# Performance work log

Measured on AMD Instinct MI355X. Metric: run time of the kernel, lower is better.

The kernel has to match this reference:

```python
import jax, jax.numpy as jnp
import numpy as np

D = 32  # per-modality feature dim (hard-coded in module)


def setup_inputs() -> dict:
    key = jax.random.key(0)
    ks = jax.random.split(key, 6)
    B, U = 16, 2048
    return {
        "a_emb": jax.random.normal(ks[0], (B, U, D), dtype=jnp.float32),
        "v_emb": jax.random.normal(ks[1], (B, U, D), dtype=jnp.float32),
        "l_emb": jax.random.normal(ks[2], (B, U, D), dtype=jnp.float32),
        "fc1_w": jax.random.normal(ks[3], (2 * D, 2 * D), dtype=jnp.float32) * 0.1,
        "fc1_b": jax.random.normal(ks[4], (2 * D,), dtype=jnp.float32) * 0.1,
        "fc2_w": jax.random.normal(ks[5], (1, 2 * D), dtype=jnp.float32) * 0.1,
    }


def _bi_attn(f1, f2):
    # f1: [B,u1,d], f2: [B,u2,d]
    B12 = jnp.einsum("bid,bjd->bij", f1, f2)          # [B,u1,u2]
    N1 = jax.nn.softmax(B12, axis=1)                    # softmax over dim=1 (as in torch code)
    N2 = jax.nn.softmax(jnp.swapaxes(B12, 1, 2), axis=1)  # B21 = B12^T
    O1 = jnp.einsum("bij,bjd->bid", N1, f2)            # [B,u1,d]
    O2 = jnp.einsum("bji,bjd->bid", jnp.swapaxes(N2, 1, 2), f1)  # [B,u2,d]
    A1 = O1 * f1
    A2 = O2 * f2
    return jnp.concatenate([A1, A2], axis=2)            # [B,u,2d]


def reference(a_emb, v_emb, l_emb, fc1_w, fc1_b, fc2_w):
    attnAV = _bi_attn(a_emb, v_emb)
    attnAL = _bi_attn(a_emb, l_emb)
    attnVL = _bi_attn(v_emb, l_emb)
    u = a_emb.shape[1]
    # The original loop recomputes the identical Bi/Ci/alpha/CCA_i every iteration
    # (always slices index 0), so compute once and repeat u times.
    Bi = jnp.concatenate(
        [attnAV[:, 0:1, :], attnAL[:, 0:1, :], attnVL[:, 0:1, :]], axis=1
    )  # [B,3,2d]
    Ci = jnp.tanh(Bi @ fc1_w.T + fc1_b) @ fc2_w.T       # [B,3,1]
    alpha = jax.nn.softmax(Ci, axis=0)                   # softmax over batch dim (as in source)
    CCA_i = jnp.einsum("bki,bkd->bid", alpha, Bi)       # [B,1,2d]
    CCA = jnp.repeat(CCA_i, u, axis=1)                   # [B,u,2d]
    return CCA
```

## Files before the change

### kernel.cpp

```cpp
#include <hip/hip_runtime.h>

#define UU 2048
#define DM 32
#define TB 128
#define NB 16
#define NP 3
#define NT (UU / TB)
#define NSTRIP 16
#define ASZ (NB * UU * DM)

#define WS_S1 0
#define WS_S2 (NP * NB * UU)
#define WS_OO (2 * NP * NB * UU)
#define WS_CCA (WS_OO + NP * NB * 2 * DM)
#define WS_SPLIT 204800

typedef short short8_t __attribute__((ext_vector_type(8)));
typedef float float4_t __attribute__((ext_vector_type(4)));

#if __has_builtin(__builtin_amdgcn_exp2f)
#define EXP2(x) __builtin_amdgcn_exp2f(x)
#else
#define EXP2(x) exp2f(x)
#endif

#define SQRT_LOG2E 1.2011224087864498f

__device__ inline void async16(void* lds, const void* g) {
  __builtin_amdgcn_global_load_lds(
      (const __attribute__((address_space(1))) unsigned int*)g,
      (__attribute__((address_space(3))) unsigned int*)lds, 16, 0, 0);
}

__device__ inline void split8s(const float4 x0, const float4 x1, short8_t& h,
                               short8_t& lo) {
  float xs[8] = {x0.x, x0.y, x0.z, x0.w, x1.x, x1.y, x1.z, x1.w};
#pragma unroll
  for (int i = 0; i < 8; ++i) {
    float xv = xs[i] * SQRT_LOG2E;
    unsigned u = __float_as_uint(xv);
    h[i] = (short)(u >> 16);
    float hif = __uint_as_float(u & 0xffff0000u);
    lo[i] = (short)(__float_as_uint(xv - hif) >> 16);
  }
}

__global__ __launch_bounds__(256) void stage0_prep(
    const float* __restrict__ a, const float* __restrict__ v,
    const float* __restrict__ l, float* __restrict__ ws) {
  const int gid = blockIdx.x * 256 + threadIdx.x;
  if (gid < (NP * NB * 2 * DM) / 4)
    ((float4*)(ws + WS_OO))[gid] = make_float4(0.f, 0.f, 0.f, 0.f);

  const int per = ASZ / 8;
  const int arr = (gid >= per) + (gid >= 2 * per);
  const float* src = (arr == 0) ? a : (arr == 1) ? v : l;
  const int loc = gid - arr * per;
  const float4* sp = (const float4*)(src + (size_t)loc * 8);
  float4 x0 = sp[0], x1 = sp[1];
  short8_t h, lo;
  split8s(x0, x1, h, lo);
  unsigned short* hq =
      (unsigned short*)(ws + WS_SPLIT) + (size_t)arr * 2 * ASZ + (size_t)loc * 8;
  *(short8_t*)hq = h;
  *(short8_t*)(hq + ASZ) = lo;
}

__global__ __launch_bounds__(256, 3) void stage1_sums(
    const unsigned short* __restrict__ H, float* __restrict__ S1part,
    float* __restrict__ S2) {
  const int lid = blockIdx.x;
  const int xcd = lid & 7;
  const int r6 = lid >> 3;
  const int z = xcd * 6 + (r6 >> 4);
  const int strip = r6 & 15;
  const int p = z >> 4, b = z & 15;
  const int i0 = strip * TB;

  const int a1 = (p == 2) ? 1 : 0;
  const int a2 = (p == 0) ? 1 : 2;
  const unsigned short* f1h = H + (size_t)a1 * 2 * ASZ + (size_t)b * UU * DM;
  const unsigned short* f2h = H + (size_t)a2 * 2 * ASZ + (size_t)b * UU * DM;

  __shared__ __align__(16) unsigned short Bbuf[2][2][TB][DM];
  __shared__ float ldsC[4][TB];
  __shared__ float S1L[UU];

  const int t = threadIdx.x;
  const int lane = t & 63, w = t >> 6;
  const int lm = lane & 15, lq = lane >> 4, k0 = lq * 8;

#pragma unroll
  for (int m = 0; m < 8; ++m) S1L[m * 256 + t] = 0.f;

  short8_t a_h[2], a_l[2];
  {
    const unsigned short* ar = f1h + (size_t)(i0 + w * 32 + lm) * DM + k0;
    a_h[0] = *(const short8_t*)ar;
    a_h[1] = *(const short8_t*)(ar + 16 * DM);
    a_l[0] = *(const short8_t*)(ar + ASZ);
    a_l[1] = *(const short8_t*)(ar + ASZ + 16 * DM);
  }

  float rowp[2][4];
#pragma unroll
  for (int rt = 0; rt < 2; ++rt)
#pragma unroll
    for (int r = 0; r < 4; ++r) rowp[rt][r] = 0.f;

  auto stageB = [&](int buf, int jt) {
    const unsigned short* gh = f2h + (size_t)(jt * TB + w * 32) * DM + lane * 8;
    async16(&Bbuf[buf][0][w * 32][0], gh);
    async16(&Bbuf[buf][0][w * 32 + 16][0], gh + 16 * DM);
    async16(&Bbuf[buf][1][w * 32][0], gh + ASZ);
    async16(&Bbuf[buf][1][w * 32 + 16][0], gh + ASZ + 16 * DM);
  };

  auto compute = [&](int buf, int jt) {
    float colp[8];
#pragma unroll
    for (int ct = 0; ct < 8; ++ct) colp[ct] = 0.f;
#pragma unroll
    for (int ct = 0; ct < 8; ++ct) {
      short8_t b_h = *(const short8_t*)&Bbuf[buf][0][ct * 16 + lm][k0];
      short8_t b_l = *(const short8_t*)&Bbuf[buf][1][ct * 16 + lm][k0];
#pragma unroll
      for (int rt = 0; rt < 2; ++rt) {
        float4_t c = {0.f, 0.f, 0.f, 0.f};
        c = __builtin_amdgcn_mfma_f32_16x16x32_bf16(a_h[rt], b_h, c, 0, 0, 0);
        c = __builtin_amdgcn_mfma_f32_16x16x32_bf16(a_h[rt], b_l, c, 0, 0, 0);
        c = __builtin_amdgcn_mfma_f32_16x16x32_bf16(a_l[rt], b_h, c, 0, 0, 0);
        float e0 = EXP2(c[0]);
        float e1 = EXP2(c[1]);
        float e2 = EXP2(c[2]);
        float e3 = EXP2(c[3]);
        rowp[rt][0] += e0;
        rowp[rt][1] += e1;
        rowp[rt][2] += e2;
        rowp[rt][3] += e3;
        colp[ct] += (e0 + e1) + (e2 + e3);
      }
    }
#pragma unroll
    for (int ct = 0; ct < 8; ++ct) {
      float vv = colp[ct];
      vv += __shfl_xor(vv, 16, 64);
      vv += __shfl_xor(vv, 32, 64);
      if (lane < 16) ldsC[w][ct * 16 + lane] = vv;
    }
    asm volatile("s_waitcnt lgkmcnt(0)" ::: "memory");
    __builtin_amdgcn_s_barrier();
    asm volatile("" ::: "memory");
    if (t < TB)
      S1L[jt * TB + t] += ldsC[0][t] + ldsC[1][t] + ldsC[2][t] + ldsC[3][t];
  };

  stageB(0, 0);

#pragma unroll 2
  for (int k = 0; k < NT; ++k) {
    if (k + 1 < NT) {
      stageB((k + 1) & 1, k + 1);
      asm volatile("s_waitcnt vmcnt(4)" ::: "memory");
    } else {
      asm volatile("s_waitcnt vmcnt(0)" ::: "memory");
    }
    __builtin_amdgcn_s_barrier();
    asm volatile("" ::: "memory");
    compute(k & 1, k);
  }
  __syncthreads();

  {
    float* dst = S1part + ((size_t)z * NSTRIP + strip) * UU;
#pragma unroll
    for (int m = 0; m < 8; ++m) dst[m * 256 + t] = S1L[m * 256 + t];
  }
  const size_t base = (size_t)z * UU;
#pragma unroll
  for (int rt = 0; rt < 2; ++rt)
#pragma unroll
    for (int r = 0; r < 4; ++r) {
      float vv = rowp[rt][r];
      vv += __shfl_xor(vv, 1, 64);
      vv += __shfl_xor(vv, 2, 64);
      vv += __shfl_xor(vv, 4, 64);
      vv += __shfl_xor(vv, 8, 64);
      if (lm == 0) S2[base + i0 + w * 32 + rt * 16 + lq * 4 + r] = vv;
    }
}

__global__ __launch_bounds__(256) void stage2_O(
    const float* __restrict__ a, const float* __restrict__ v,
    const float* __restrict__ l, const float* __restrict__ S1part,
    const float* __restrict__ S2, float* __restrict__ OO) {
  const int idx = blockIdx.x;
  const int chunk = idx & 7;
  const int pd = idx >> 3;
  const int dir = pd & 1;
  const int pb = pd >> 1;
  const int p = pb >> 4, b = pb & 15;
  const float* f1 = (p == 2) ? v : a;
  const float* f2 = (p == 0) ? v : l;
  f1 += (size_t)b * UU * DM;
  f2 += (size_t)b * UU * DM;
  const float* qrow = (dir == 0) ? f1 : f2;
  const float* rows = (dir == 0) ? f2 : f1;

  __shared__ float qv[DM];
  __shared__ __align__(16) float rowsL[256 * 36];
  __shared__ float wL[256];
  __shared__ float wred[8][DM];
  const int t = threadIdx.x;
  if (t < DM) qv[t] = qrow[t];
  __syncthreads();

  const int r = chunk * 256 + t;
  const float4* rp = (const float4*)(rows + (size_t)r * DM);
  float dot = 0.f;
#pragma unroll
  for (int qq = 0; qq < 8; ++qq) {
    float4 x = rp[qq];
    *(float4*)&rowsL[t * 36 + qq * 4] = x;
    dot = fmaf(x.x, qv[4 * qq + 0], dot);
    dot = fmaf(x.y, qv[4 * qq + 1], dot);
    dot = fmaf(x.z, qv[4 * qq + 2], dot);
    dot = fmaf(x.w, qv[4 * qq + 3], dot);
  }
  float den;
  if (dir == 0) {
    const float* sp = S1part + (size_t)pb * NSTRIP * UU + r;
    float s = 0.f;
#pragma unroll
    for (int s16 = 0; s16 < NSTRIP; ++s16) s += sp[(size_t)s16 * UU];
    den = s;
  } else {
    den = S2[(size_t)pb * UU + r];
  }
  wL[t] = __expf(dot) / den;
  __syncthreads();

  const int d = t & 31, sl = t >> 5;
  float acc = 0.f;
#pragma unroll
  for (int k = 0; k < 32; ++k) {
    const int rr = sl * 32 + k;
    acc = fmaf(wL[rr], rowsL[rr * 36 + d], acc);
  }
  wred[sl][d] = acc;
  __syncthreads();
  if (t < DM) {
    float o = 0.f;
#pragma unroll
    for (int s2 = 0; s2 < 8; ++s2) o += wred[s2][t];
    atomicAdd(&OO[(size_t)pd * DM + t], o);
  }
}

__global__ __launch_bounds__(1024) void stage3_head(
    const float* __restrict__ a, const float* __restrict__ v,
    const float* __restrict__ l, const float* __restrict__ OO,
    const float* __restrict__ fc1w, const float* __restrict__ fc1b,
    const float* __restrict__ fc2w, float* __restrict__ CCA) {
  const int t = threadIdx.x;
  __shared__ float BiL[NB * NP * 64];
  __shared__ float CiS[NB * NP];
  __shared__ float denomk[NP];
  __shared__ float fwL[64 * 65];

#pragma unroll
  for (int it = 0; it < 4; ++it) {
    int m = it * 1024 + t;
    fwL[(m >> 6) * 65 + (m & 63)] = fc1w[m];
  }

#pragma unroll
  for (int iter = 0; iter < 3; ++iter) {
    int m = iter * 1024 + t;
    int bk = m >> 6;
    int h = m & 63;
    int b = bk / NP, p = bk - b * NP;
    int dir = h >> 5, hd = h & 31;
    const float* base = (dir == 0) ? ((p == 2) ? v : a) : ((p == 0) ? v : l);
    float q = base[(size_t)b * UU * DM + hd];
    int pb = p * NB + b;
    BiL[bk * 64 + h] = OO[(pb * 2 + dir) * DM + hd] * q;
  }
  __syncthreads();

  const int h = t & 63;
  const int g = t >> 6;
#pragma unroll
  for (int iter = 0; iter < 3; ++iter) {
    int bk = g + 16 * iter;
    float x = fc1b[h];
#pragma unroll 8
    for (int c = 0; c < 64; ++c)
      x = fmaf(BiL[bk * 64 + c], fwL[h * 65 + c], x);
    float vv = tanhf(x) * fc2w[h];
#pragma unroll
    for (int off = 32; off > 0; off >>= 1) vv += __shfl_down(vv, off, 64);
    if (h == 0) CiS[bk] = vv;
  }
  __syncthreads();

  if (t < NP) {
    float s = 0.f;
    for (int b = 0; b < NB; ++b) s += __expf(CiS[b * NP + t]);
    denomk[t] = s;
  }
  __syncthreads();

  {
    int b = g;
    float s = 0.f;
#pragma unroll
    for (int k = 0; k < NP; ++k)
      s += __expf(CiS[b * NP + k]) / denomk[k] * BiL[(b * NP + k) * 64 + h];
    CCA[b * 64 + h] = s;
  }
}

__global__ __launch_bounds__(256) void stage4_bcast(
    const float* __restrict__ CCA, float4* __restrict__ out) {
  const int gid = blockIdx.x * 256 + threadIdx.x;
  const int c4 = gid & 15;
  const int b = gid >> 15;
  const float4* cc = (const float4*)CCA;
  out[gid] = cc[b * 16 + c4];
}

extern "C" void kernel_launch(void* const* d_in, const int* in_sizes, int n_in,
                              void* d_out, int out_size, void* d_ws,
                              size_t ws_size, hipStream_t stream) {
  const float* a = (const float*)d_in[0];
  const float* v = (const float*)d_in[1];
  const float* l = (const float*)d_in[2];
  const float* fc1w = (const float*)d_in[3];
  const float* fc1b = (const float*)d_in[4];
  const float* fc2w = (const float*)d_in[5];
  float* out = (float*)d_out;

  float* ws = (float*)d_ws;
  float* S2 = ws + WS_S2;
  float* OO = ws + WS_OO;
  float* CCA = ws + WS_CCA;
  const unsigned short* H = (const unsigned short*)(ws + WS_SPLIT);
  float* S1part = (float*)d_out;

  stage0_prep<<<dim3(1536), 256, 0, stream>>>(a, v, l, ws);
  stage1_sums<<<dim3(NP * NB * NSTRIP), 256, 0, stream>>>(H, S1part, S2);
  stage2_O<<<dim3(NP * NB * 2 * 8), 256, 0, stream>>>(a, v, l, S1part, S2, OO);
  stage3_head<<<dim3(1), 1024, 0, stream>>>(a, v, l, OO, fc1w, fc1b, fc2w,
                                            CCA);
  stage4_bcast<<<dim3(2048), 256, 0, stream>>>(CCA, (float4*)out);
}
```

Before: 147.1 us.

## Split stage1 work by column tile per wave to drop per-tile barriers

Stage1 previously gave each wave 32 rows of the query strip and staged shared B tiles through LDS with async loads, needing a block barrier every tile to combine column sums. Now each wave holds all 128 query rows in registers and loads its own 32 B columns straight from global memory into registers, double-buffered. Each wave then owns distinct S1L entries, so the per-tile barrier and LDS reduction go away, and a single final LDS reduction combines row sums across waves. This raises register pressure (8 A fragments plus 8x4 row accumulators) and drops LDS reuse of B across waves, which may hurt occupancy under launch_bounds(256,3).

```diff
diff --git a/kernel.cpp b/kernel.cpp
--- a/kernel.cpp
+++ b/kernel.cpp
@@ -25,12 +25,6 @@
 #endif
 
 #define SQRT_LOG2E 1.2011224087864498f
-
-__device__ inline void async16(void* lds, const void* g) {
-  __builtin_amdgcn_global_load_lds(
-      (const __attribute__((address_space(1))) unsigned int*)g,
-      (__attribute__((address_space(3))) unsigned int*)lds, 16, 0, 0);
-}
 
 __device__ inline void split8s(const float4 x0, const float4 x1, short8_t& h,
                                short8_t& lo) {
@@ -82,50 +76,55 @@
   const unsigned short* f1h = H + (size_t)a1 * 2 * ASZ + (size_t)b * UU * DM;
   const unsigned short* f2h = H + (size_t)a2 * 2 * ASZ + (size_t)b * UU * DM;
 
-  __shared__ __align__(16) unsigned short Bbuf[2][2][TB][DM];
-  __shared__ float ldsC[4][TB];
   __shared__ float S1L[UU];
+  __shared__ float S2L[4][TB];
 
   const int t = threadIdx.x;
   const int lane = t & 63, w = t >> 6;
   const int lm = lane & 15, lq = lane >> 4, k0 = lq * 8;
 
 #pragma unroll
-  for (int m = 0; m < 8; ++m) S1L[m * 256 + t] = 0.f;
-
-  short8_t a_h[2], a_l[2];
-  {
-    const unsigned short* ar = f1h + (size_t)(i0 + w * 32 + lm) * DM + k0;
-    a_h[0] = *(const short8_t*)ar;
-    a_h[1] = *(const short8_t*)(ar + 16 * DM);
-    a_l[0] = *(const short8_t*)(ar + ASZ);
-    a_l[1] = *(const short8_t*)(ar + ASZ + 16 * DM);
-  }
-
-  float rowp[2][4];
-#pragma unroll
-  for (int rt = 0; rt < 2; ++rt)
+  for (int m = 0; m < 8; ++m) {
+    int jt = m * 2 + (lane >> 5);
+    S1L[jt * TB + w * 32 + (lane & 31)] = 0.f;
+  }
+
+  short8_t a_h[8], a_l[8];
+#pragma unroll
+  for (int rt = 0; rt < 8; ++rt) {
+    const unsigned short* ar = f1h + (size_t)(i0 + rt * 16 + lm) * DM + k0;
+    a_h[rt] = *(const short8_t*)ar;
+    a_l[rt] = *(const short8_t*)(ar + ASZ);
+  }
+
+  float rowp[8][4];
+#pragma unroll
+  for (int rt = 0; rt < 8; ++rt)
 #pragma unroll
     for (int r = 0; r < 4; ++r) rowp[rt][r] = 0.f;
 
-  auto stageB = [&](int buf, int jt) {
-    const unsigned short* gh = f2h + (size_t)(jt * TB + w * 32) * DM + lane * 8;
-    async16(&Bbuf[buf][0][w * 32][0], gh);
-    async16(&Bbuf[buf][0][w * 32 + 16][0], gh + 16 * DM);
-    async16(&Bbuf[buf][1][w * 32][0], gh + ASZ);
-    async16(&Bbuf[buf][1][w * 32 + 16][0], gh + ASZ + 16 * DM);
+  short8_t bh[2][2], bl[2][2];
+  const unsigned short* gb0 = f2h + (size_t)(w * 32 + lm) * DM + k0;
+  auto loadB = [&](int jt, int s) {
+    const unsigned short* gb = gb0 + (size_t)jt * TB * DM;
+    bh[s][0] = *(const short8_t*)gb;
+    bh[s][1] = *(const short8_t*)(gb + 16 * DM);
+    bl[s][0] = *(const short8_t*)(gb + ASZ);
+    bl[s][1] = *(const short8_t*)(gb + ASZ + 16 * DM);
   };
 
-  auto compute = [&](int buf, int jt) {
-    float colp[8];
-#pragma unroll
-    for (int ct = 0; ct < 8; ++ct) colp[ct] = 0.f;
-#pragma unroll
-    for (int ct = 0; ct < 8; ++ct) {
-      short8_t b_h = *(const short8_t*)&Bbuf[buf][0][ct * 16 + lm][k0];
-      short8_t b_l = *(const short8_t*)&Bbuf[buf][1][ct * 16 + lm][k0];
-#pragma unroll
-      for (int rt = 0; rt < 2; ++rt) {
+  loadB(0, 0);
+#pragma unroll 2
+  for (int k = 0; k < NT; ++k) {
+    const int cur = k & 1;
+    if (k + 1 < NT) loadB(k + 1, cur ^ 1);
+#pragma unroll
+    for (int ct = 0; ct < 2; ++ct) {
+      const short8_t b_h = bh[cur][ct];
+      const short8_t b_l = bl[cur][ct];
+      float colp = 0.f;
+#pragma unroll
+      for (int rt = 0; rt < 8; ++rt) {
         float4_t c = {0.f, 0.f, 0.f, 0.f};
         c = __builtin_amdgcn_mfma_f32_16x16x32_bf16(a_h[rt], b_h, c, 0, 0, 0);
         c = __builtin_amdgcn_mfma_f32_16x16x32_bf16(a_h[rt], b_l, c, 0, 0, 0);
@@ -138,47 +137,16 @@
         rowp[rt][1] += e1;
         rowp[rt][2] += e2;
         rowp[rt][3] += e3;
-        colp[ct] += (e0 + e1) + (e2 + e3);
+        colp += (e0 + e1) + (e2 + e3);
       }
+      colp += __shfl_xor(colp, 16, 64);
+      colp += __shfl_xor(colp, 32, 64);
+      if (lane < 16) S1L[k * TB + w * 32 + ct * 16 + lane] += colp;
     }
-#pragma unroll
-    for (int ct = 0; ct < 8; ++ct) {
-      float vv = colp[ct];
-      vv += __shfl_xor(vv, 16, 64);
-      vv += __shfl_xor(vv, 32, 64);
-      if (lane < 16) ldsC[w][ct * 16 + lane] = vv;
-    }
-    asm volatile("s_waitcnt lgkmcnt(0)" ::: "memory");
-    __builtin_amdgcn_s_barrier();
-    asm volatile("" ::: "memory");
-    if (t < TB)
-      S1L[jt * TB + t] += ldsC[0][t] + ldsC[1][t] + ldsC[2][t] + ldsC[3][t];
-  };
-
-  stageB(0, 0);
-
-#pragma unroll 2
-  for (int k = 0; k < NT; ++k) {
-    if (k + 1 < NT) {
-      stageB((k + 1) & 1, k + 1);
-      asm volatile("s_waitcnt vmcnt(4)" ::: "memory");
-    } else {
-      asm volatile("s_waitcnt vmcnt(0)" ::: "memory");
-    }
-    __builtin_amdgcn_s_barrier();
-    asm volatile("" ::: "memory");
-    compute(k & 1, k);
-  }
-  __syncthreads();
-
-  {
-    float* dst = S1part + ((size_t)z * NSTRIP + strip) * UU;
-#pragma unroll
-    for (int m = 0; m < 8; ++m) dst[m * 256 + t] = S1L[m * 256 + t];
-  }
-  const size_t base = (size_t)z * UU;
-#pragma unroll
-  for (int rt = 0; rt < 2; ++rt)
+  }
+
+#pragma unroll
+  for (int rt = 0; rt < 8; ++rt)
 #pragma unroll
     for (int r = 0; r < 4; ++r) {
       float vv = rowp[rt][r];
@@ -186,8 +154,19 @@
       vv += __shfl_xor(vv, 2, 64);
       vv += __shfl_xor(vv, 4, 64);
       vv += __shfl_xor(vv, 8, 64);
-      if (lm == 0) S2[base + i0 + w * 32 + rt * 16 + lq * 4 + r] = vv;
+      if (lm == 0) S2L[w][rt * 16 + lq * 4 + r] = vv;
     }
+  __syncthreads();
+
+  const size_t base = (size_t)z * UU;
+  if (t < TB)
+    S2[base + i0 + t] = S2L[0][t] + S2L[1][t] + S2L[2][t] + S2L[3][t];
+
+  {
+    float* dst = S1part + ((size_t)z * NSTRIP + strip) * UU;
+#pragma unroll
+    for (int m = 0; m < 8; ++m) dst[m * 256 + t] = S1L[m * 256 + t];
+  }
 }
 
 __global__ __launch_bounds__(256) void stage2_O(
```

Result: slower. 329.5 us (+124.1%).

## Fuse head computation into broadcast kernel, recomputing head redundantly per block

Applied to the files above, without the earlier changes.

The single-block head kernel and the broadcast kernel are merged into one 2048-block kernel. Each block recomputes the whole tiny MLP head (fc1, tanh, fc2, batch softmax) into shared memory and then writes its slice of the broadcast output. This removes one kernel launch and the serial single-block stage, at the cost of redundant head work and extra fc1_w/OO reads in every block.

```diff
diff --git a/kernel.cpp b/kernel.cpp
--- a/kernel.cpp
+++ b/kernel.cpp
@@ -12,7 +12,6 @@
 #define WS_S1 0
 #define WS_S2 (NP * NB * UU)
 #define WS_OO (2 * NP * NB * UU)
-#define WS_CCA (WS_OO + NP * NB * 2 * DM)
 #define WS_SPLIT 204800
 
 typedef short short8_t __attribute__((ext_vector_type(8)));
@@ -257,47 +256,53 @@
   }
 }
 
-__global__ __launch_bounds__(1024) void stage3_head(
+__global__ __launch_bounds__(256) void stage4_head_bcast(
     const float* __restrict__ a, const float* __restrict__ v,
     const float* __restrict__ l, const float* __restrict__ OO,
     const float* __restrict__ fc1w, const float* __restrict__ fc1b,
-    const float* __restrict__ fc2w, float* __restrict__ CCA) {
-  const int t = threadIdx.x;
+    const float* __restrict__ fc2w, float4* __restrict__ out) {
+  __shared__ float fwL[64 * 65];
   __shared__ float BiL[NB * NP * 64];
   __shared__ float CiS[NB * NP];
   __shared__ float denomk[NP];
-  __shared__ float fwL[64 * 65];
-
-#pragma unroll
-  for (int it = 0; it < 4; ++it) {
-    int m = it * 1024 + t;
+  __shared__ __align__(16) float ccaL[64];
+  const int t = threadIdx.x;
+  const int myb = blockIdx.x >> 7;
+
+#pragma unroll
+  for (int it = 0; it < 16; ++it) {
+    int m = it * 256 + t;
     fwL[(m >> 6) * 65 + (m & 63)] = fc1w[m];
   }
-
-#pragma unroll
-  for (int iter = 0; iter < 3; ++iter) {
-    int m = iter * 1024 + t;
+#pragma unroll
+  for (int it = 0; it < 12; ++it) {
+    int m = it * 256 + t;
     int bk = m >> 6;
-    int h = m & 63;
-    int b = bk / NP, p = bk - b * NP;
-    int dir = h >> 5, hd = h & 31;
-    const float* base = (dir == 0) ? ((p == 2) ? v : a) : ((p == 0) ? v : l);
-    float q = base[(size_t)b * UU * DM + hd];
-    int pb = p * NB + b;
-    BiL[bk * 64 + h] = OO[(pb * 2 + dir) * DM + hd] * q;
+    int h2 = m & 63;
+    int b2 = bk / NP, p2 = bk - b2 * NP;
+    int dir2 = h2 >> 5, hd = h2 & 31;
+    const float* base2 =
+        (dir2 == 0) ? ((p2 == 2) ? v : a) : ((p2 == 0) ? v : l);
+    float q = base2[(size_t)b2 * UU * DM + hd];
+    int pb2 = p2 * NB + b2;
+    BiL[bk * 64 + h2] = OO[(pb2 * 2 + dir2) * DM + hd] * q;
   }
   __syncthreads();
 
   const int h = t & 63;
   const int g = t >> 6;
 #pragma unroll
-  for (int iter = 0; iter < 3; ++iter) {
-    int bk = g + 16 * iter;
-    float x = fc1b[h];
-#pragma unroll 8
-    for (int c = 0; c < 64; ++c)
-      x = fmaf(BiL[bk * 64 + c], fwL[h * 65 + c], x);
-    float vv = tanhf(x) * fc2w[h];
+  for (int it = 0; it < 12; ++it) {
+    int bk = g + 4 * it;
+    float x0 = 0.f, x1 = 0.f, x2 = 0.f, x3 = 0.f;
+#pragma unroll
+    for (int c = 0; c < 16; ++c) {
+      x0 = fmaf(BiL[bk * 64 + c], fwL[h * 65 + c], x0);
+      x1 = fmaf(BiL[bk * 64 + 16 + c], fwL[h * 65 + 16 + c], x1);
+      x2 = fmaf(BiL[bk * 64 + 32 + c], fwL[h * 65 + 32 + c], x2);
+      x3 = fmaf(BiL[bk * 64 + 48 + c], fwL[h * 65 + 48 + c], x3);
+    }
+    float vv = tanhf(((x0 + x1) + (x2 + x3)) + fc1b[h]) * fc2w[h];
 #pragma unroll
     for (int off = 32; off > 0; off >>= 1) vv += __shfl_down(vv, off, 64);
     if (h == 0) CiS[bk] = vv;
@@ -306,28 +311,23 @@
 
   if (t < NP) {
     float s = 0.f;
-    for (int b = 0; b < NB; ++b) s += __expf(CiS[b * NP + t]);
+    for (int b2 = 0; b2 < NB; ++b2) s += __expf(CiS[b2 * NP + t]);
     denomk[t] = s;
   }
   __syncthreads();
 
-  {
-    int b = g;
+  if (t < 64) {
     float s = 0.f;
 #pragma unroll
     for (int k = 0; k < NP; ++k)
-      s += __expf(CiS[b * NP + k]) / denomk[k] * BiL[(b * NP + k) * 64 + h];
-    CCA[b * 64 + h] = s;
-  }
-}
-
-__global__ __launch_bounds__(256) void stage4_bcast(
-    const float* __restrict__ CCA, float4* __restrict__ out) {
-  const int gid = blockIdx.x * 256 + threadIdx.x;
-  const int c4 = gid & 15;
-  const int b = gid >> 15;
-  const float4* cc = (const float4*)CCA;
-  out[gid] = cc[b * 16 + c4];
+      s += __expf(CiS[myb * NP + k]) / denomk[k] *
+           BiL[(myb * NP + k) * 64 + t];
+    ccaL[t] = s;
+  }
+  __syncthreads();
+
+  const int gid = blockIdx.x * 256 + t;
+  out[gid] = ((const float4*)ccaL)[t & 15];
 }
 
 extern "C" void kernel_launch(void* const* d_in, const int* in_sizes, int n_in,
@@ -344,14 +344,12 @@
   float* ws = (float*)d_ws;
   float* S2 = ws + WS_S2;
   float* OO = ws + WS_OO;
-  float* CCA = ws + WS_CCA;
   const unsigned short* H = (const unsigned short*)(ws + WS_SPLIT);
   float* S1part = (float*)d_out;
 
   stage0_prep<<<dim3(1536), 256, 0, stream>>>(a, v, l, ws);
   stage1_sums<<<dim3(NP * NB * NSTRIP), 256, 0, stream>>>(H, S1part, S2);
   stage2_O<<<dim3(NP * NB * 2 * 8), 256, 0, stream>>>(a, v, l, S1part, S2, OO);
-  stage3_head<<<dim3(1), 1024, 0, stream>>>(a, v, l, OO, fc1w, fc1b, fc2w,
-                                            CCA);
-  stage4_bcast<<<dim3(2048), 256, 0, stream>>>(CCA, (float4*)out);
-}
+  stage4_head_bcast<<<dim3(2048), 256, 0, stream>>>(a, v, l, OO, fc1w, fc1b,
+                                                    fc2w, (float4*)out);
+}
```

Measured after the change: 189.3 us. 28.7% more time.
